# Performance work log

Hardware: AMD Instinct MI355X
Metric: run time of the kernel (lower is better)

## Reference

```python
import jax, jax.numpy as jnp
import numpy as np

B, Q, K, D, H = 16, 128, 128, 512, 512
NEG = -1e6


def setup_inputs() -> dict:
    key = jax.random.key(0)
    ks = jax.random.split(key, 7)
    return {
        "queries": jax.random.normal(ks[0], (B, Q, D), dtype=jnp.float32),
        "keys": jax.random.normal(ks[1], (B, K, D), dtype=jnp.float32),
        "values": jax.random.normal(ks[2], (B, K, D), dtype=jnp.float32),
        "valid_lens": jax.random.randint(ks[3], (B,), 1, K + 1, dtype=jnp.int32),
        "Wq": jax.random.normal(ks[4], (D, H), dtype=jnp.float32) / np.sqrt(D),
        "Wk": jax.random.normal(ks[5], (D, H), dtype=jnp.float32) / np.sqrt(D),
        "wv": jax.random.normal(ks[6], (H,), dtype=jnp.float32) / np.sqrt(H),
    }


def reference(queries, keys, values, valid_lens, Wq, Wk, wv):
    # projections (LazyLinear, bias=False)
    q = jnp.einsum("bqd,dh->bqh", queries, Wq)  # [B,Q,H]
    k = jnp.einsum("bkd,dh->bkh", keys, Wk)    # [B,K,H]
    # broadcast add -> tanh -> reduce to scalar score (Bahdanau)
    feats = jnp.tanh(q[:, :, None, :] + k[:, None, :, :])  # [B,Q,K,H]
    scores = jnp.einsum("bqkh,h->bqk", feats, wv)           # [B,Q,K]
    # masked softmax over key dim using per-batch valid lengths
    mask = jnp.arange(scores.shape[-1])[None, None, :] < valid_lens[:, None, None]
    scores = jnp.where(mask, scores, NEG)
    attn = jax.nn.softmax(scores, axis=-1)                  # [B,Q,K]
    # dropout is identity in eval mode
    return jnp.einsum("bqk,bkv->bqv", attn, values)
```

## Files before the change

### kernel.cpp

```cpp
#include <hip/hip_runtime.h>

#define Bn 16
#define Qn 128
#define Kn 128
#define Dn 512
#define Hn 512
#define NEGV (-3.0e38f)
#define PSCALE 2.8853900817779268f

typedef short s16x8 __attribute__((ext_vector_type(8)));
typedef float f32x4 __attribute__((ext_vector_type(4)));

__device__ __forceinline__ float exp2_hw(float x) {
  float r;
  asm("v_exp_f32 %0, %1" : "=v"(r) : "v"(x));
  return r;
}
__device__ __forceinline__ unsigned short f2bf(float f) {
  unsigned int u = __float_as_uint(f);
  u += 0x7fff + ((u >> 16) & 1);
  return (unsigned short)(u >> 16);
}
__device__ __forceinline__ float bf_lo(unsigned int u) { return __uint_as_float(u << 16); }
__device__ __forceinline__ float bf_hi(unsigned int u) { return __uint_as_float(u & 0xffff0000u); }

__global__ __launch_bounds__(256) void convert_kernel(
    const float* __restrict__ queries, const float* __restrict__ keys,
    const float* __restrict__ Wq, const float* __restrict__ Wk,
    const float* __restrict__ values,
    unsigned short* __restrict__ Abf, unsigned short* __restrict__ Wt,
    unsigned short* __restrict__ Vt)
{
  const int bid = blockIdx.x, t = threadIdx.x;
  if (bid < 512) {
    const int gid = bid * 256 + t;
    const size_t base = (size_t)gid * 16;
    const float* src = (base < 1048576) ? (queries + base) : (keys + (base - 1048576));
    unsigned short o[16];
    #pragma unroll
    for (int j = 0; j < 4; ++j) {
      float4 v = *(const float4*)(src + j * 4);
      o[j * 4 + 0] = f2bf(v.x); o[j * 4 + 1] = f2bf(v.y);
      o[j * 4 + 2] = f2bf(v.z); o[j * 4 + 3] = f2bf(v.w);
    }
    #pragma unroll
    for (int j = 0; j < 4; ++j)
      *(ushort4*)(Abf + base + j * 4) = *(ushort4*)&o[j * 4];
  } else if (bid < 640) {
    const int tid = (bid - 512) * 256 + t;
    const int n = tid & 511, rest = tid >> 9;
    const int sel = rest >> 5, k16 = rest & 31;
    const float* W = sel ? Wk : Wq;
    unsigned short o[16];
    #pragma unroll
    for (int i = 0; i < 16; ++i)
      o[i] = f2bf(W[(size_t)(k16 * 16 + i) * Hn + n]);
    unsigned short* dst = Wt + (size_t)sel * 262144 + (size_t)n * 512 + k16 * 16;
    #pragma unroll
    for (int j = 0; j < 4; ++j) *(ushort4*)(dst + j * 4) = *(ushort4*)&o[j * 4];
  } else {
    const int tid = (bid - 640) * 256 + t;
    const int d = tid & 511, rest = tid >> 9;
    const int b = rest >> 2, k32 = rest & 3;
    unsigned short o[32];
    #pragma unroll
    for (int i = 0; i < 32; ++i)
      o[i] = f2bf(values[((size_t)(b * Kn + k32 * 32 + i)) * Dn + d]);
    unsigned short* dst = Vt + (size_t)b * 65536 + (size_t)d * 128 + k32 * 32;
    #pragma unroll
    for (int j = 0; j < 8; ++j) *(ushort4*)(dst + j * 4) = *(ushort4*)&o[j * 4];
  }
}

__global__ __launch_bounds__(256) void proj_mfma(
    const unsigned short* __restrict__ Abf, const unsigned short* __restrict__ Wt,
    float* __restrict__ Eq, unsigned short* __restrict__ Ek)
{
  __shared__ unsigned short Al[128][72];
  __shared__ unsigned short Bl[64][72];
  const int t = threadIdx.x, w = t >> 6, l = t & 63;
  const int wm = w >> 1, wn = w & 1;
  const int rowTile = blockIdx.x;
  const int n0 = blockIdx.y * 64;
  const int R0 = rowTile * 128;
  const bool isQ = rowTile < 16;
  const unsigned short* Wsel = Wt + (isQ ? 0 : 262144);

  f32x4 acc[4][2];
  #pragma unroll
  for (int m = 0; m < 4; ++m)
    #pragma unroll
    for (int n = 0; n < 2; ++n) acc[m][n] = (f32x4)0.f;

  const int lr = l & 15, lk = l >> 4;

  for (int k0 = 0; k0 < Hn; k0 += 64) {
    ushort4 ar[4][2], br[2][2];
    #pragma unroll
    for (int i = 0; i < 4; ++i) {
      int g = t + 256 * i, r = g >> 3, c = g & 7;
      const unsigned short* p = Abf + (size_t)(R0 + r) * Hn + k0 + c * 8;
      ar[i][0] = *(const ushort4*)p; ar[i][1] = *(const ushort4*)(p + 4);
    }
    #pragma unroll
    for (int i = 0; i < 2; ++i) {
      int g = t + 256 * i, r = g >> 3, c = g & 7;
      const unsigned short* p = Wsel + (size_t)(n0 + r) * Hn + k0 + c * 8;
      br[i][0] = *(const ushort4*)p; br[i][1] = *(const ushort4*)(p + 4);
    }
    __syncthreads();
    #pragma unroll
    for (int i = 0; i < 4; ++i) {
      int g = t + 256 * i, r = g >> 3, c = g & 7;
      *(ushort4*)&Al[r][c * 8] = ar[i][0]; *(ushort4*)&Al[r][c * 8 + 4] = ar[i][1];
    }
    #pragma unroll
    for (int i = 0; i < 2; ++i) {
      int g = t + 256 * i, r = g >> 3, c = g & 7;
      *(ushort4*)&Bl[r][c * 8] = br[i][0]; *(ushort4*)&Bl[r][c * 8 + 4] = br[i][1];
    }
    __syncthreads();
    #pragma unroll
    for (int ks = 0; ks < 2; ++ks) {
      s16x8 af[4], bf_[2];
      #pragma unroll
      for (int m = 0; m < 4; ++m)
        af[m] = *(const s16x8*)&Al[wm * 64 + m * 16 + lr][ks * 32 + lk * 8];
      #pragma unroll
      for (int n = 0; n < 2; ++n)
        bf_[n] = *(const s16x8*)&Bl[wn * 32 + n * 16 + lr][ks * 32 + lk * 8];
      #pragma unroll
      for (int m = 0; m < 4; ++m)
        #pragma unroll
        for (int n = 0; n < 2; ++n)
          acc[m][n] = __builtin_amdgcn_mfma_f32_16x16x32_bf16(af[m], bf_[n], acc[m][n], 0, 0, 0);
    }
    __syncthreads();
  }

  #pragma unroll
  for (int m = 0; m < 4; ++m)
    #pragma unroll
    for (int n = 0; n < 2; ++n)
      #pragma unroll
      for (int r = 0; r < 4; ++r) {
        int row = R0 + wm * 64 + m * 16 + lk * 4 + r;
        int col = n0 + wn * 32 + n * 16 + lr;
        float e = exp2_hw(acc[m][n][r] * PSCALE);
        if (isQ) Eq[(size_t)row * Hn + col] = e;
        else     Ek[(size_t)(row - 2048) * Hn + col] = f2bf(e);
      }
}

__global__ __launch_bounds__(256) void score_kernel(
    const float* __restrict__ Eq, const unsigned short* __restrict__ Ek,
    const float* __restrict__ wv, const int* __restrict__ valid_lens,
    unsigned short* __restrict__ At)
{
  __shared__ unsigned short EkL[128][68];
  __shared__ float EqL[2][72];
  __shared__ float WVL[512];
  __shared__ float Red[4];

  const int t = threadIdx.x;
  const int b = blockIdx.y;
  const int q0 = blockIdx.x * 2;
  const int q_loc = t >> 7, kk = t & 127;

  if (t < 128) {
    float4 w4 = *(const float4*)(wv + t * 4);
    w4.x *= -2.f; w4.y *= -2.f; w4.z *= -2.f; w4.w *= -2.f;
    *(float4*)&WVL[t * 4] = w4;
  }

  uint2 ekr[8];
  float4 eqr = {0.f, 0.f, 0.f, 0.f};
  const unsigned short* Ekb = Ek + (size_t)b * Kn * Hn;

  auto prefetch = [&](int c) {
    #pragma unroll
    for (int i = 0; i < 8; ++i) {
      int g = t + 256 * i, r = g >> 4, c4 = g & 15;
      ekr[i] = *(const uint2*)(Ekb + (size_t)r * Hn + c * 64 + c4 * 4);
    }
    if (t < 32) {
      int r = t >> 4, c4 = t & 15;
      eqr = *(const float4*)(Eq + ((size_t)(b * Qn + q0 + r)) * Hn + c * 64 + c4 * 4);
    }
  };

  prefetch(0);
  float acc = 0.f;

  for (int c = 0; c < 8; ++c) {
    __syncthreads();
    #pragma unroll
    for (int i = 0; i < 8; ++i) {
      int g = t + 256 * i, r = g >> 4, c4 = g & 15;
      *(uint2*)&EkL[r][c4 * 4] = ekr[i];
    }
    if (t < 32) {
      int r = t >> 4, c4 = t & 15;
      *(float4*)&EqL[r][c4 * 4] = eqr;
    }
    if (c < 7) prefetch(c + 1);
    __syncthreads();

    #pragma unroll
    for (int h8 = 0; h8 < 8; ++h8) {
      uint2 e0 = *(const uint2*)&EkL[kk][h8 * 8];
      uint2 e1 = *(const uint2*)&EkL[kk][h8 * 8 + 4];
      float4 qa = *(const float4*)&EqL[q_loc][h8 * 8];
      float4 qb = *(const float4*)&EqL[q_loc][h8 * 8 + 4];
      float4 wa = *(const float4*)&WVL[c * 64 + h8 * 8];
      float4 wb = *(const float4*)&WVL[c * 64 + h8 * 8 + 4];
      float A, B, num, den;
      A = __builtin_fmaf(qa.x, bf_lo(e0.x), 1.f);
      B = __builtin_fmaf(qa.y, bf_hi(e0.x), 1.f);
      num = __builtin_fmaf(wa.y, A, wa.x * B);
      den = A * B;
      acc = __builtin_fmaf(num, __builtin_amdgcn_rcpf(den), acc);
      A = __builtin_fmaf(qa.z, bf_lo(e0.y), 1.f);
      B = __builtin_fmaf(qa.w, bf_hi(e0.y), 1.f);
      num = __builtin_fmaf(wa.w, A, wa.z * B);
      den = A * B;
      acc = __builtin_fmaf(num, __builtin_amdgcn_rcpf(den), acc);
      A = __builtin_fmaf(qb.x, bf_lo(e1.x), 1.f);
      B = __builtin_fmaf(qb.y, bf_hi(e1.x), 1.f);
      num = __builtin_fmaf(wb.y, A, wb.x * B);
      den = A * B;
      acc = __builtin_fmaf(num, __builtin_amdgcn_rcpf(den), acc);
      A = __builtin_fmaf(qb.z, bf_lo(e1.y), 1.f);
      B = __builtin_fmaf(qb.w, bf_hi(e1.y), 1.f);
      num = __builtin_fmaf(wb.w, A, wb.z * B);
      den = A * B;
      acc = __builtin_fmaf(num, __builtin_amdgcn_rcpf(den), acc);
    }
  }

  const int vlen = valid_lens[b];
  const bool ok = kk < vlen;
  const int w = t >> 6;
  float sv = ok ? acc : NEGV;
  #pragma unroll
  for (int xm = 32; xm >= 1; xm >>= 1) sv = fmaxf(sv, __shfl_xor(sv, xm));
  if ((t & 63) == 0) Red[w] = sv;
  __syncthreads();
  float m = fmaxf(sv, Red[w ^ 1]);
  float ev = ok ? exp2_hw((acc - m) * 1.44269504f) : 0.f;
  float s = ev;
  #pragma unroll
  for (int xm = 32; xm >= 1; xm >>= 1) s += __shfl_xor(s, xm);
  __syncthreads();
  if ((t & 63) == 0) Red[w] = s;
  __syncthreads();
  float sum = s + Red[w ^ 1];
  At[((size_t)(b * Qn) + q0 + q_loc) * Kn + kk] = f2bf(ev * __builtin_amdgcn_rcpf(sum));
}

__global__ __launch_bounds__(256) void av_mfma(
    const unsigned short* __restrict__ At, const unsigned short* __restrict__ Vt,
    float* __restrict__ out)
{
  __shared__ unsigned short AtL[128][72];
  __shared__ unsigned short VL[128][72];
  const int t = threadIdx.x, w = t >> 6, l = t & 63;
  const int wm = w >> 1, wn = w & 1;
  const int dt = blockIdx.x;
  const int b = blockIdx.y;
  const int lr = l & 15, lk = l >> 4;

  f32x4 acc[4][4];
  #pragma unroll
  for (int m = 0; m < 4; ++m)
    #pragma unroll
    for (int n = 0; n < 4; ++n) acc[m][n] = (f32x4)0.f;

  const unsigned short* Atb = At + (size_t)b * Qn * Kn;
  const unsigned short* Vtb = Vt + (size_t)b * 65536 + (size_t)dt * 128 * Kn;

  for (int k0 = 0; k0 < Kn; k0 += 64) {
    ushort4 ar[4][2], vr[4][2];
    #pragma unroll
    for (int i = 0; i < 4; ++i) {
      int g = t + 256 * i, r = g >> 3, c = g & 7;
      const unsigned short* p = Atb + (size_t)r * Kn + k0 + c * 8;
      ar[i][0] = *(const ushort4*)p; ar[i][1] = *(const ushort4*)(p + 4);
      const unsigned short* pv = Vtb + (size_t)r * Kn + k0 + c * 8;
      vr[i][0] = *(const ushort4*)pv; vr[i][1] = *(const ushort4*)(pv + 4);
    }
    __syncthreads();
    #pragma unroll
    for (int i = 0; i < 4; ++i) {
      int g = t + 256 * i, r = g >> 3, c = g & 7;
      *(ushort4*)&AtL[r][c * 8] = ar[i][0]; *(ushort4*)&AtL[r][c * 8 + 4] = ar[i][1];
      *(ushort4*)&VL[r][c * 8] = vr[i][0];  *(ushort4*)&VL[r][c * 8 + 4] = vr[i][1];
    }
    __syncthreads();
    #pragma unroll
    for (int ks = 0; ks < 2; ++ks) {
      s16x8 af[4], bf_[4];
      #pragma unroll
      for (int m = 0; m < 4; ++m)
        af[m] = *(const s16x8*)&AtL[wm * 64 + m * 16 + lr][ks * 32 + lk * 8];
      #pragma unroll
      for (int n = 0; n < 4; ++n)
        bf_[n] = *(const s16x8*)&VL[wn * 64 + n * 16 + lr][ks * 32 + lk * 8];
      #pragma unroll
      for (int m = 0; m < 4; ++m)
        #pragma unroll
        for (int n = 0; n < 4; ++n)
          acc[m][n] = __builtin_amdgcn_mfma_f32_16x16x32_bf16(af[m], bf_[n], acc[m][n], 0, 0, 0);
    }
    __syncthreads();
  }

  #pragma unroll
  for (int m = 0; m < 4; ++m)
    #pragma unroll
    for (int n = 0; n < 4; ++n)
      #pragma unroll
      for (int r = 0; r < 4; ++r) {
        int row = wm * 64 + m * 16 + lk * 4 + r;
        int col = dt * 128 + wn * 64 + n * 16 + lr;
        out[((size_t)(b * Qn) + row) * Dn + col] = acc[m][n][r];
      }
}

extern "C" void kernel_launch(void* const* d_in, const int* in_sizes, int n_in,
                              void* d_out, int out_size, void* d_ws, size_t ws_size,
                              hipStream_t stream) {
  const float* queries    = (const float*)d_in[0];
  const float* keys       = (const float*)d_in[1];
  const float* values     = (const float*)d_in[2];
  const int*   valid_lens = (const int*)d_in[3];
  const float* Wq         = (const float*)d_in[4];
  const float* Wk         = (const float*)d_in[5];
  const float* wv         = (const float*)d_in[6];
  float* out = (float*)d_out;

  unsigned short* Abf = (unsigned short*)d_ws;
  unsigned short* Wt  = Abf + 2097152;
  unsigned short* Vt  = Wt + 524288;
  float*          Eq  = (float*)(Vt + 1048576);
  unsigned short* Ek  = (unsigned short*)(Eq + 1048576);
  unsigned short* At  = Ek + 1048576;

  convert_kernel<<<768, 256, 0, stream>>>(queries, keys, Wq, Wk, values, Abf, Wt, Vt);
  proj_mfma<<<dim3(32, 8), 256, 0, stream>>>(Abf, Wt, Eq, Ek);
  score_kernel<<<dim3(64, 16), 256, 0, stream>>>(Eq, Ek, wv, valid_lens, At);
  av_mfma<<<dim3(4, 16), 256, 0, stream>>>(At, Vt, out);
}
```

Before: 50.46 us.

## Precompute weighted exp(-q) terms and transpose fp32 Ek for wider score blocks

The projection epilogue now writes exp(-2q) together with a wv-scaled copy as interleaved float2 pairs. It also stores exp(2k) in fp32, transposed so pairs of hidden columns are contiguous per key. The score kernel reads the query terms straight from global memory with uniform per-wave addresses and drops its staging of Eq and wv through LDS. It also processes 4 queries per 512-thread block, reusing each Ek tile across more queries and cutting the bf16 unpack work. In exchange, Ek traffic doubles from bf16 to fp32, the scattered transposed stores in the projection epilogue are less coalesced, and the QW buffer is twice as large.

```diff
diff --git a/kernel.cpp b/kernel.cpp
--- a/kernel.cpp
+++ b/kernel.cpp
@@ -21,8 +21,6 @@
   u += 0x7fff + ((u >> 16) & 1);
   return (unsigned short)(u >> 16);
 }
-__device__ __forceinline__ float bf_lo(unsigned int u) { return __uint_as_float(u << 16); }
-__device__ __forceinline__ float bf_hi(unsigned int u) { return __uint_as_float(u & 0xffff0000u); }
 
 __global__ __launch_bounds__(256) void convert_kernel(
     const float* __restrict__ queries, const float* __restrict__ keys,
@@ -74,7 +72,8 @@
 
 __global__ __launch_bounds__(256) void proj_mfma(
     const unsigned short* __restrict__ Abf, const unsigned short* __restrict__ Wt,
-    float* __restrict__ Eq, unsigned short* __restrict__ Ek)
+    const float* __restrict__ wv,
+    float* __restrict__ QW, float* __restrict__ Ekt)
 {
   __shared__ unsigned short Al[128][72];
   __shared__ unsigned short Bl[64][72];
@@ -146,115 +145,82 @@
       for (int r = 0; r < 4; ++r) {
         int row = R0 + wm * 64 + m * 16 + lk * 4 + r;
         int col = n0 + wn * 32 + n * 16 + lr;
-        float e = exp2_hw(acc[m][n][r] * PSCALE);
-        if (isQ) Eq[(size_t)row * Hn + col] = e;
-        else     Ek[(size_t)(row - 2048) * Hn + col] = f2bf(e);
+        float a = acc[m][n][r];
+        if (isQ) {
+          float F  = exp2_hw(-PSCALE * a);
+          float WF = -2.f * wv[col] * F;
+          float2 o = {WF, F};
+          *(float2*)(QW + ((size_t)row * Hn + col) * 2) = o;
+        } else {
+          int krow = row - 2048;
+          int bb = krow >> 7, k = krow & 127;
+          float e = exp2_hw(PSCALE * a);
+          Ekt[((size_t)(bb * 256 + (col >> 1)) * 128 + k) * 2 + (col & 1)] = e;
+        }
       }
 }
 
-__global__ __launch_bounds__(256) void score_kernel(
-    const float* __restrict__ Eq, const unsigned short* __restrict__ Ek,
-    const float* __restrict__ wv, const int* __restrict__ valid_lens,
-    unsigned short* __restrict__ At)
+__global__ __launch_bounds__(512) void score_kernel(
+    const float* __restrict__ QW, const float* __restrict__ Ekt,
+    const int* __restrict__ valid_lens, unsigned short* __restrict__ At)
 {
-  __shared__ unsigned short EkL[128][68];
-  __shared__ float EqL[2][72];
-  __shared__ float WVL[512];
-  __shared__ float Red[4];
+  __shared__ float EkL[8192];
+  __shared__ float RedM[4][2], RedS[4][2];
 
   const int t = threadIdx.x;
   const int b = blockIdx.y;
-  const int q0 = blockIdx.x * 2;
-  const int q_loc = t >> 7, kk = t & 127;
-
-  if (t < 128) {
-    float4 w4 = *(const float4*)(wv + t * 4);
-    w4.x *= -2.f; w4.y *= -2.f; w4.z *= -2.f; w4.w *= -2.f;
-    *(float4*)&WVL[t * 4] = w4;
-  }
-
-  uint2 ekr[8];
-  float4 eqr = {0.f, 0.f, 0.f, 0.f};
-  const unsigned short* Ekb = Ek + (size_t)b * Kn * Hn;
-
-  auto prefetch = [&](int c) {
-    #pragma unroll
-    for (int i = 0; i < 8; ++i) {
-      int g = t + 256 * i, r = g >> 4, c4 = g & 15;
-      ekr[i] = *(const uint2*)(Ekb + (size_t)r * Hn + c * 64 + c4 * 4);
-    }
-    if (t < 32) {
-      int r = t >> 4, c4 = t & 15;
-      eqr = *(const float4*)(Eq + ((size_t)(b * Qn + q0 + r)) * Hn + c * 64 + c4 * 4);
-    }
-  };
-
-  prefetch(0);
+  const int q0 = blockIdx.x * 4;
+  const int kk = t & 127;
+  const int hf = (t >> 6) & 1;
+  const int q_loc = __builtin_amdgcn_readfirstlane(t >> 7);
+
+  const float* qw = QW + (size_t)(b * Qn + q0 + q_loc) * 1024;
+  const float4* src = (const float4*)(Ekt + (size_t)b * 65536);
+
+  float4 pr[4];
+  #pragma unroll
+  for (int j = 0; j < 4; ++j) pr[j] = src[t + j * 512];
+
   float acc = 0.f;
-
   for (int c = 0; c < 8; ++c) {
     __syncthreads();
     #pragma unroll
-    for (int i = 0; i < 8; ++i) {
-      int g = t + 256 * i, r = g >> 4, c4 = g & 15;
-      *(uint2*)&EkL[r][c4 * 4] = ekr[i];
-    }
-    if (t < 32) {
-      int r = t >> 4, c4 = t & 15;
-      *(float4*)&EqL[r][c4 * 4] = eqr;
-    }
-    if (c < 7) prefetch(c + 1);
-    __syncthreads();
-
-    #pragma unroll
-    for (int h8 = 0; h8 < 8; ++h8) {
-      uint2 e0 = *(const uint2*)&EkL[kk][h8 * 8];
-      uint2 e1 = *(const uint2*)&EkL[kk][h8 * 8 + 4];
-      float4 qa = *(const float4*)&EqL[q_loc][h8 * 8];
-      float4 qb = *(const float4*)&EqL[q_loc][h8 * 8 + 4];
-      float4 wa = *(const float4*)&WVL[c * 64 + h8 * 8];
-      float4 wb = *(const float4*)&WVL[c * 64 + h8 * 8 + 4];
-      float A, B, num, den;
-      A = __builtin_fmaf(qa.x, bf_lo(e0.x), 1.f);
-      B = __builtin_fmaf(qa.y, bf_hi(e0.x), 1.f);
-      num = __builtin_fmaf(wa.y, A, wa.x * B);
-      den = A * B;
-      acc = __builtin_fmaf(num, __builtin_amdgcn_rcpf(den), acc);
-      A = __builtin_fmaf(qa.z, bf_lo(e0.y), 1.f);
-      B = __builtin_fmaf(qa.w, bf_hi(e0.y), 1.f);
-      num = __builtin_fmaf(wa.w, A, wa.z * B);
-      den = A * B;
-      acc = __builtin_fmaf(num, __builtin_amdgcn_rcpf(den), acc);
-      A = __builtin_fmaf(qb.x, bf_lo(e1.x), 1.f);
-      B = __builtin_fmaf(qb.y, bf_hi(e1.x), 1.f);
-      num = __builtin_fmaf(wb.y, A, wb.x * B);
-      den = A * B;
-      acc = __builtin_fmaf(num, __builtin_amdgcn_rcpf(den), acc);
-      A = __builtin_fmaf(qb.z, bf_lo(e1.y), 1.f);
-      B = __builtin_fmaf(qb.w, bf_hi(e1.y), 1.f);
-      num = __builtin_fmaf(wb.w, A, wb.z * B);
-      den = A * B;
-      acc = __builtin_fmaf(num, __builtin_amdgcn_rcpf(den), acc);
+    for (int j = 0; j < 4; ++j) ((float4*)EkL)[t + j * 512] = pr[j];
+    if (c < 7) {
+      const float4* s2 = src + (c + 1) * 2048;
+      #pragma unroll
+      for (int j = 0; j < 4; ++j) pr[j] = s2[t + j * 512];
+    }
+    __syncthreads();
+
+    const float* qc = qw + c * 128;
+    #pragma unroll
+    for (int i = 0; i < 32; ++i) {
+      float4 qv = *(const float4*)(qc + 4 * i);
+      float2 ek = *(const float2*)&EkL[i * 256 + 2 * kk];
+      float d0 = qv.y + ek.x;
+      float d1 = qv.w + ek.y;
+      float num = __builtin_fmaf(qv.x, d1, qv.z * d0);
+      float dd = d0 * d1;
+      acc = __builtin_fmaf(num, __builtin_amdgcn_rcpf(dd), acc);
     }
   }
 
   const int vlen = valid_lens[b];
   const bool ok = kk < vlen;
-  const int w = t >> 6;
   float sv = ok ? acc : NEGV;
   #pragma unroll
   for (int xm = 32; xm >= 1; xm >>= 1) sv = fmaxf(sv, __shfl_xor(sv, xm));
-  if ((t & 63) == 0) Red[w] = sv;
+  if ((t & 63) == 0) RedM[q_loc][hf] = sv;
   __syncthreads();
-  float m = fmaxf(sv, Red[w ^ 1]);
+  float m = fmaxf(RedM[q_loc][0], RedM[q_loc][1]);
   float ev = ok ? exp2_hw((acc - m) * 1.44269504f) : 0.f;
   float s = ev;
   #pragma unroll
   for (int xm = 32; xm >= 1; xm >>= 1) s += __shfl_xor(s, xm);
+  if ((t & 63) == 0) RedS[q_loc][hf] = s;
   __syncthreads();
-  if ((t & 63) == 0) Red[w] = s;
-  __syncthreads();
-  float sum = s + Red[w ^ 1];
+  float sum = RedS[q_loc][0] + RedS[q_loc][1];
   At[((size_t)(b * Qn) + q0 + q_loc) * Kn + kk] = f2bf(ev * __builtin_amdgcn_rcpf(sum));
 }
 
@@ -342,12 +308,12 @@
   unsigned short* Abf = (unsigned short*)d_ws;
   unsigned short* Wt  = Abf + 2097152;
   unsigned short* Vt  = Wt + 524288;
-  float*          Eq  = (float*)(Vt + 1048576);
-  unsigned short* Ek  = (unsigned short*)(Eq + 1048576);
-  unsigned short* At  = Ek + 1048576;
+  float*          QW  = (float*)(Vt + 1048576);
+  float*          Ekt = QW + 2097152;
+  unsigned short* At  = (unsigned short*)(Ekt + 1048576);
 
   convert_kernel<<<768, 256, 0, stream>>>(queries, keys, Wq, Wk, values, Abf, Wt, Vt);
-  proj_mfma<<<dim3(32, 8), 256, 0, stream>>>(Abf, Wt, Eq, Ek);
-  score_kernel<<<dim3(64, 16), 256, 0, stream>>>(Eq, Ek, wv, valid_lens, At);
+  proj_mfma<<<dim3(32, 8), 256, 0, stream>>>(Abf, Wt, wv, QW, Ekt);
+  score_kernel<<<dim3(32, 16), 512, 0, stream>>>(QW, Ekt, valid_lens, At);
   av_mfma<<<dim3(4, 16), 256, 0, stream>>>(At, Vt, out);
 }
```

Measured after the change: 82.28 us. 63.1% more time.
